# Kernel optimization log

Measured on AMD Instinct MI355X. Metric: run time of the kernel, lower is better.

Reference implementation:

```python
import jax, jax.numpy as jnp
import numpy as np
import math

L, H, P = 16384, 128, 256


def setup_inputs() -> dict:
    key = jax.random.key(0)
    k = jax.random.split(key, 6)
    return {
        "input_sequence": jax.random.normal(k[0], (L, H), dtype=jnp.float32),
        "A_diag": jax.random.uniform(k[1], (P,), dtype=jnp.float32),
        "B": (jax.random.uniform(k[2], (P, H, 2), dtype=jnp.float32) * 2.0 - 1.0) / math.sqrt(H),
        "C": (jax.random.uniform(k[3], (H, P, 2), dtype=jnp.float32) * 2.0 - 1.0) / math.sqrt(P),
        "D": jax.random.normal(k[4], (H,), dtype=jnp.float32),
        "steps": jax.random.uniform(k[5], (P,), dtype=jnp.float32),
    }


def _binop(qi, qj):
    # 2x2 block-diagonal matrix product + affine state propagation, per channel.
    iA, iB, iC, iD, ib1, ib2 = qi
    jA, jB, jC, jD, jb1, jb2 = qj
    return (
        jA * iA + jB * iC,
        jA * iB + jB * iD,
        jC * iA + jD * iC,
        jC * iB + jD * iD,
        jA * ib1 + jB * ib2 + jb1,
        jC * ib1 + jD * ib2 + jb2,
    )


def reference(input_sequence, A_diag, B, C, D, steps):
    # LinOSS-IM discretization (implicit)
    A = jax.nn.relu(A_diag)                      # (P,)
    dt = jax.nn.sigmoid(steps)                   # (P,)
    Bc = B[..., 0] + 1j * B[..., 1]              # (P,H) complex64
    Cc = C[..., 0] + 1j * C[..., 1]              # (H,P) complex64

    Bu = input_sequence @ Bc.T                   # (L,P) complex64

    schur = 1.0 / (1.0 + dt ** 2 * A)
    M11 = 1.0 - dt ** 2 * A * schur
    M12 = -dt * A * schur
    M21 = dt * schur
    M22 = schur

    ones = jnp.ones((input_sequence.shape[0], A.shape[0]), dtype=input_sequence.dtype)
    F1 = M11 * Bu * dt                           # (L,P) complex
    F2 = M21 * Bu * dt

    elems = (M11 * ones, M12 * ones, M21 * ones, M22 * ones, F1, F2)
    _, _, _, _, _, x2 = jax.lax.associative_scan(_binop, elems)  # scan over L

    ys = jnp.real(x2 @ Cc.T)                     # (L,H)
    return ys + input_sequence * D
```

## Files before the change

### kernel.cpp

```cpp
#include <hip/hip_runtime.h>
#include <math.h>

#define L 16384
#define H 128
#define P 256
#define CL 64
#define NCH (L/CL)
#define GS 16
#define NG (NCH/GS)
#define KDIM 512
#define NBU 512

typedef __attribute__((ext_vector_type(8))) short short8;
typedef __attribute__((ext_vector_type(4))) float f32x4;

__device__ inline unsigned short f2bf(float f){
  union { float f; unsigned u; } v; v.f = f;
  unsigned u = v.u;
  u += 0x7fffu + ((u >> 16) & 1u);
  return (unsigned short)(u >> 16);
}
__device__ inline float bf2f(unsigned short s){
  union { unsigned u; float f; } v; v.u = ((unsigned)s) << 16;
  return v.f;
}

struct Params { float M11,M12,M21,M22,s1,s2; };

__device__ inline Params get_params(const float* A_diag, const float* steps, int p){
  float A = A_diag[p]; A = A > 0.f ? A : 0.f;
  float dt = 1.f/(1.f + expf(-steps[p]));
  float schur = 1.f/(1.f + dt*dt*A);
  Params q;
  q.M11 = 1.f - dt*dt*A*schur;
  q.M12 = -dt*A*schur;
  q.M21 = dt*schur;
  q.M22 = schur;
  q.s1 = q.M11*dt;
  q.s2 = q.M21*dt;
  return q;
}

__device__ inline unsigned long long aload(const unsigned long long* p){
  return __hip_atomic_load((unsigned long long*)p, __ATOMIC_RELAXED,
                           __HIP_MEMORY_SCOPE_AGENT);
}
__device__ inline void apub(unsigned long long* p, unsigned long long v){
  (void)__hip_atomic_exchange(p, v, __ATOMIC_RELAXED, __HIP_MEMORY_SCOPE_AGENT);
}
__device__ inline void fpub(unsigned* p){
  (void)__hip_atomic_exchange(p, 1u, __ATOMIC_RELAXED, __HIP_MEMORY_SCOPE_AGENT);
}
__device__ inline void wait_flag(unsigned* f){
  while (__hip_atomic_load(f, __ATOMIC_RELAXED, __HIP_MEMORY_SCOPE_AGENT) == 0u)
    __builtin_amdgcn_s_sleep(1);
}

__global__ __launch_bounds__(512) void prep_w(const float* __restrict__ B,
                                              const float* __restrict__ Cw,
                                              unsigned short* __restrict__ BWswz,
                                              unsigned short* __restrict__ Bswz,
                                              unsigned* __restrict__ flags){
  int gidx = blockIdx.x*512 + threadIdx.x;
  if (gidx < NCH + NG) flags[gidx] = 0u;
  if (gidx < H*NBU){
    int k = gidx >> 9, n = gidx & 511;
    int p = n & 255, c2 = n >> 8;
    float v = B[((size_t)p*H + k)*2 + c2];
    BWswz[((size_t)(k>>3)*NBU + n)*8 + (k&7)] = f2bf(v);
  } else {
    int g2 = gidx - H*NBU;
    int k = g2 >> 7, n = g2 & 127;
    float v = (k < P) ? Cw[((size_t)n*P + k)*2]
                      : -Cw[((size_t)n*P + (k-P))*2 + 1];
    Bswz[((size_t)(k>>3)*H + n)*8 + (k&7)] = f2bf(v);
  }
}

__global__ __launch_bounds__(512, 2) void linoss_fused(
    const float* __restrict__ in,
    const float* __restrict__ A_diag,
    const float* __restrict__ steps,
    const float* __restrict__ Dv,
    const unsigned short* __restrict__ BWswz,
    const unsigned short* __restrict__ Bswz,
    unsigned long long* __restrict__ finals,
    unsigned long long* __restrict__ gfin,
    unsigned* __restrict__ flag1,
    unsigned* __restrict__ flag2,
    float* __restrict__ out)
{
  __shared__ unsigned short sX[CL][NBU+8];
  const int c   = blockIdx.x;
  const int tid = threadIdx.x;

  {
    int lane = tid & 63, w = tid >> 6;
    int ml = lane & 15, quad = lane >> 4;
    int rt = w & 3, ch = w >> 2;
    int lm0 = rt*16;
    const float* aptr = in + (size_t)(c*CL + lm0 + ml)*H + quad*8;
    short8 av[4];
    #pragma unroll
    for (int ks=0; ks<4; ks++){
      float4 f0 = *(const float4*)(aptr + ks*32);
      float4 f1 = *(const float4*)(aptr + ks*32 + 4);
      union { short8 s; unsigned short u[8]; } o;
      o.u[0]=f2bf(f0.x); o.u[1]=f2bf(f0.y); o.u[2]=f2bf(f0.z); o.u[3]=f2bf(f0.w);
      o.u[4]=f2bf(f1.x); o.u[5]=f2bf(f1.y); o.u[6]=f2bf(f1.z); o.u[7]=f2bf(f1.w);
      av[ks] = o.s;
    }
    f32x4 acc[16];
    #pragma unroll
    for (int t=0;t<16;t++) acc[t] = (f32x4){0.f,0.f,0.f,0.f};
    #pragma unroll
    for (int ks=0; ks<4; ks++){
      #pragma unroll
      for (int t=0;t<16;t++){
        int n0 = ch*256 + t*16;
        short8 bv = *(const short8*)(BWswz + ((size_t)(ks*4+quad)*NBU + n0 + ml)*8);
        acc[t] = __builtin_amdgcn_mfma_f32_16x16x32_bf16(av[ks], bv, acc[t], 0, 0, 0);
      }
    }
    #pragma unroll
    for (int t=0;t<16;t++){
      int n = ch*256 + t*16 + ml;
      #pragma unroll
      for (int r=0;r<4;r++)
        sX[lm0 + quad*4 + r][n] = f2bf(acc[t][r]);
    }
  }
  __syncthreads();

  const int p = tid & 255, part = tid >> 8;
  Params q = get_params(A_diag, steps, p);
  float Ta=q.M11, Tb=q.M12, Tc=q.M21, Td=q.M22;
  #pragma unroll
  for (int s=0;s<6;s++){
    float na=Ta*Ta+Tb*Tc, nb=Ta*Tb+Tb*Td, nc=Tc*Ta+Td*Tc, nd=Tc*Tb+Td*Td;
    Ta=na;Tb=nb;Tc=nc;Td=nd;
  }
  float fx1=0.f, fx2=0.f;
  {
    #pragma unroll
    for (int i=0;i<CL;i++){
      float u = bf2f(sX[i][part*256 + p]);
      float n1 = q.M11*fx1 + q.M12*fx2 + q.s1*u;
      float n2 = q.M21*fx1 + q.M22*fx2 + q.s2*u;
      fx1 = n1; fx2 = n2;
    }
    union { unsigned long long u; float2 f; } w; w.f = make_float2(fx1,fx2);
    apub(&finals[(size_t)(part*NCH + c)*P + p], w.u);
  }
  asm volatile("s_waitcnt vmcnt(0)" ::: "memory");
  __syncthreads();
  if (tid == 0) fpub(&flag1[c]);

  const int g = c >> 4, iw = c & (GS-1);
  const unsigned long long* Fp = finals + (size_t)part*NCH*P + (size_t)g*GS*P + p;

  float z1=0.f, z2v=0.f;
  bool have_z = false;
  if (iw == GS-1){
    if (tid < GS-1) wait_flag(&flag1[g*GS + tid]);
    __syncthreads();
    unsigned long long v[GS-1];
    #pragma unroll
    for (int j=0;j<GS-1;j++) v[j] = aload(Fp + (size_t)j*P);
    #pragma unroll
    for (int j=0;j<GS-1;j++){
      union { unsigned long long u; float2 f; } w; w.u = v[j];
      float n1 = Ta*z1 + Tb*z2v + w.f.x;
      float n2 = Tc*z1 + Td*z2v + w.f.y;
      z1=n1; z2v=n2;
    }
    have_z = true;
    float t1 = Ta*z1 + Tb*z2v + fx1;
    float t2 = Tc*z1 + Td*z2v + fx2;
    union { unsigned long long u; float2 f; } w; w.f = make_float2(t1,t2);
    apub(&gfin[(size_t)(part*NG + g)*P + p], w.u);
    asm volatile("s_waitcnt vmcnt(0)" ::: "memory");
    __syncthreads();
    if (tid == 0) fpub(&flag2[g]);
  }

  float sa=1.f, sb=0.f, sc=0.f, sd=1.f;
  {
    float wa=Ta, wb=Tb, wc=Tc, wd=Td;
    #pragma unroll
    for (int bit=0; bit<4; bit++){
      if ((iw>>bit)&1){
        float na = wa*sa + wb*sc, nb = wa*sb + wb*sd;
        float nc = wc*sa + wd*sc, nd = wc*sb + wd*sd;
        sa=na; sb=nb; sc=nc; sd=nd;
      }
      float qa = wa*wa + wb*wc, qb = wa*wb + wb*wd;
      float qc = wc*wa + wd*wc, qd = wc*wb + wd*wd;
      wa=qa; wb=qb; wc=qc; wd=qd;
    }
  }
  float ga=Ta, gb=Tb, gc=Tc, gd=Td;
  #pragma unroll
  for (int s=0;s<4;s++){
    float na=ga*ga+gb*gc, nb=ga*gb+gb*gd, nc=gc*ga+gd*gc, nd=gc*gb+gd*gd;
    ga=na;gb=nb;gc=nc;gd=nd;
  }

  if (tid < g)                             wait_flag(&flag2[tid]);
  if (!have_z && tid >= 64 && tid < 64+iw) wait_flag(&flag1[g*GS + (tid-64)]);
  __syncthreads();

  {
    const unsigned long long* Gp = gfin + (size_t)part*NG*P + p;
    unsigned long long vy[NG-1], vm[GS-1];
    #pragma unroll
    for (int j=0;j<NG-1;j++) vy[j] = (j < g) ? aload(Gp + (size_t)j*P) : 0ULL;
    if (!have_z){
      #pragma unroll
      for (int j=0;j<GS-1;j++) vm[j] = (j < iw) ? aload(Fp + (size_t)j*P) : 0ULL;
    }
    float y1=0.f, y2=0.f;
    #pragma unroll
    for (int j=0;j<NG-1;j++){
      if (j < g){
        union { unsigned long long u; float2 f; } w; w.u = vy[j];
        float n1 = ga*y1 + gb*y2 + w.f.x;
        float n2 = gc*y1 + gd*y2 + w.f.y;
        y1=n1; y2=n2;
      }
    }
    if (!have_z){
      #pragma unroll
      for (int j=0;j<GS-1;j++){
        if (j < iw){
          union { unsigned long long u; float2 f; } w; w.u = vm[j];
          float n1 = Ta*z1 + Tb*z2v + w.f.x;
          float n2 = Tc*z1 + Td*z2v + w.f.y;
          z1=n1; z2v=n2;
        }
      }
    }
    float x1 = sa*y1 + sb*y2 + z1;
    float x2 = sc*y1 + sd*y2 + z2v;
    #pragma unroll
    for (int i=0;i<CL;i++){
      float u = bf2f(sX[i][part*256 + p]);
      float n1 = q.M11*x1 + q.M12*x2 + q.s1*u;
      float n2 = q.M21*x1 + q.M22*x2 + q.s2*u;
      x1 = n1; x2 = n2;
      sX[i][part*256 + p] = f2bf(x2);
    }
  }
  __syncthreads();

  {
    int lane = tid & 63, w = tid >> 6;
    int ml = lane & 15, quad = lane >> 4;
    int rt2 = w & 3;
    int nh  = w >> 2;
    f32x4 acc[4];
    #pragma unroll
    for (int j=0;j<4;j++) acc[j] = (f32x4){0.f,0.f,0.f,0.f};
    for (int ks=0; ks<KDIM/32; ks++){
      short8 av = *(const short8*)&sX[rt2*16 + ml][ks*32 + quad*8];
      #pragma unroll
      for (int j=0;j<4;j++){
        short8 bv = *(const short8*)(Bswz + ((size_t)(ks*4+quad)*H + (nh*4+j)*16 + ml)*8);
        acc[j] = __builtin_amdgcn_mfma_f32_16x16x32_bf16(av, bv, acc[j], 0, 0, 0);
      }
    }
    #pragma unroll
    for (int j=0;j<4;j++){
      int h = (nh*4+j)*16 + ml;
      float dv = Dv[h];
      #pragma unroll
      for (int r=0;r<4;r++){
        int l = c*CL + rt2*16 + quad*4 + r;
        out[(size_t)l*H + h] = acc[j][r] + in[(size_t)l*H + h]*dv;
      }
    }
  }
}

extern "C" void kernel_launch(void* const* d_in, const int* in_sizes, int n_in,
                              void* d_out, int out_size, void* d_ws, size_t ws_size,
                              hipStream_t stream) {
  const float* in     = (const float*)d_in[0];
  const float* A_diag = (const float*)d_in[1];
  const float* B      = (const float*)d_in[2];
  const float* Cw     = (const float*)d_in[3];
  const float* Dv     = (const float*)d_in[4];
  const float* steps  = (const float*)d_in[5];
  float* out = (float*)d_out;

  unsigned short* BWswz = (unsigned short*)d_ws;
  unsigned short* Bswz  = BWswz + (size_t)H*NBU;
  unsigned long long* finals = (unsigned long long*)(Bswz + (size_t)KDIM*H);
  unsigned long long* gfin   = finals + (size_t)2*NCH*P;
  unsigned* flags = (unsigned*)(gfin + (size_t)2*NG*P);
  unsigned* flag1 = flags;
  unsigned* flag2 = flags + NCH;

  prep_w<<<256, 512, 0, stream>>>(B, Cw, BWswz, Bswz, flags);
  linoss_fused<<<NCH, 512, 0, stream>>>(in, A_diag, steps, Dv, BWswz, Bswz,
                                        finals, gfin, flag1, flag2, out);
}
```

Measured before the change: 94.36 us.

## Split fused scan kernel into two launches, replacing inter-block flag synchronization

Replaces the single persistent kernel, which coordinated chunk carries through atomic flags and a two-level group scan, with two kernels. The first computes Bu via MFMA, writes it to global memory as bf16 along with per-chunk final states. The second reloads Bu, serially folds all previous chunk finals (linear in chunk index) to get its carry-in, then rescans and projects. This removes spin-waits and flag traffic but adds an extra launch, a round trip of an 8MB Bu buffer through memory, and O(NCH) serial carry work for late blocks.

```diff
diff --git a/kernel.cpp b/kernel.cpp
--- a/kernel.cpp
+++ b/kernel.cpp
@@ -6,8 +6,6 @@
 #define P 256
 #define CL 64
 #define NCH (L/CL)
-#define GS 16
-#define NG (NCH/GS)
 #define KDIM 512
 #define NBU 512
 
@@ -41,28 +39,11 @@
   return q;
 }
 
-__device__ inline unsigned long long aload(const unsigned long long* p){
-  return __hip_atomic_load((unsigned long long*)p, __ATOMIC_RELAXED,
-                           __HIP_MEMORY_SCOPE_AGENT);
-}
-__device__ inline void apub(unsigned long long* p, unsigned long long v){
-  (void)__hip_atomic_exchange(p, v, __ATOMIC_RELAXED, __HIP_MEMORY_SCOPE_AGENT);
-}
-__device__ inline void fpub(unsigned* p){
-  (void)__hip_atomic_exchange(p, 1u, __ATOMIC_RELAXED, __HIP_MEMORY_SCOPE_AGENT);
-}
-__device__ inline void wait_flag(unsigned* f){
-  while (__hip_atomic_load(f, __ATOMIC_RELAXED, __HIP_MEMORY_SCOPE_AGENT) == 0u)
-    __builtin_amdgcn_s_sleep(1);
-}
-
 __global__ __launch_bounds__(512) void prep_w(const float* __restrict__ B,
                                               const float* __restrict__ Cw,
                                               unsigned short* __restrict__ BWswz,
-                                              unsigned short* __restrict__ Bswz,
-                                              unsigned* __restrict__ flags){
+                                              unsigned short* __restrict__ Bswz){
   int gidx = blockIdx.x*512 + threadIdx.x;
-  if (gidx < NCH + NG) flags[gidx] = 0u;
   if (gidx < H*NBU){
     int k = gidx >> 9, n = gidx & 511;
     int p = n & 255, c2 = n >> 8;
@@ -77,18 +58,13 @@
   }
 }
 
-__global__ __launch_bounds__(512, 2) void linoss_fused(
+__global__ __launch_bounds__(512, 2) void k1_bu(
     const float* __restrict__ in,
     const float* __restrict__ A_diag,
     const float* __restrict__ steps,
-    const float* __restrict__ Dv,
     const unsigned short* __restrict__ BWswz,
-    const unsigned short* __restrict__ Bswz,
-    unsigned long long* __restrict__ finals,
-    unsigned long long* __restrict__ gfin,
-    unsigned* __restrict__ flag1,
-    unsigned* __restrict__ flag2,
-    float* __restrict__ out)
+    unsigned short* __restrict__ Bu,
+    float* __restrict__ finals)
 {
   __shared__ unsigned short sX[CL][NBU+8];
   const int c   = blockIdx.x;
@@ -132,6 +108,51 @@
   }
   __syncthreads();
 
+  {
+    int row = tid >> 3, seg = tid & 7;
+    const short8* src = (const short8*)&sX[row][seg*64];
+    short8* dst = (short8*)(Bu + ((size_t)(c*CL + row)*NBU + seg*64));
+    #pragma unroll
+    for (int j=0;j<8;j++) dst[j] = src[j];
+  }
+
+  {
+    const int p = tid & 255, part = tid >> 8;
+    Params q = get_params(A_diag, steps, p);
+    float fx1=0.f, fx2=0.f;
+    #pragma unroll
+    for (int i=0;i<CL;i++){
+      float u = bf2f(sX[i][part*256 + p]);
+      float n1 = q.M11*fx1 + q.M12*fx2 + q.s1*u;
+      float n2 = q.M21*fx1 + q.M22*fx2 + q.s2*u;
+      fx1 = n1; fx2 = n2;
+    }
+    ((float2*)finals)[(size_t)(part*NCH + c)*P + p] = make_float2(fx1,fx2);
+  }
+}
+
+__global__ __launch_bounds__(512, 2) void k2_out(
+    const float* __restrict__ in,
+    const float* __restrict__ A_diag,
+    const float* __restrict__ steps,
+    const float* __restrict__ Dv,
+    const unsigned short* __restrict__ Bswz,
+    const unsigned short* __restrict__ Bu,
+    const float* __restrict__ finals,
+    float* __restrict__ out)
+{
+  __shared__ unsigned short sX[CL][NBU+8];
+  const int c   = blockIdx.x;
+  const int tid = threadIdx.x;
+
+  const int row = tid >> 3, seg = tid & 7;
+  short8 st[8];
+  {
+    const short8* src = (const short8*)(Bu + ((size_t)(c*CL + row)*NBU + seg*64));
+    #pragma unroll
+    for (int j=0;j<8;j++) st[j] = src[j];
+  }
+
   const int p = tid & 255, part = tid >> 8;
   Params q = get_params(A_diag, steps, p);
   float Ta=q.M11, Tb=q.M12, Tc=q.M21, Td=q.M22;
@@ -140,108 +161,36 @@
     float na=Ta*Ta+Tb*Tc, nb=Ta*Tb+Tb*Td, nc=Tc*Ta+Td*Tc, nd=Tc*Tb+Td*Td;
     Ta=na;Tb=nb;Tc=nc;Td=nd;
   }
-  float fx1=0.f, fx2=0.f;
-  {
-    #pragma unroll
-    for (int i=0;i<CL;i++){
-      float u = bf2f(sX[i][part*256 + p]);
-      float n1 = q.M11*fx1 + q.M12*fx2 + q.s1*u;
-      float n2 = q.M21*fx1 + q.M22*fx2 + q.s2*u;
-      fx1 = n1; fx2 = n2;
-    }
-    union { unsigned long long u; float2 f; } w; w.f = make_float2(fx1,fx2);
-    apub(&finals[(size_t)(part*NCH + c)*P + p], w.u);
-  }
-  asm volatile("s_waitcnt vmcnt(0)" ::: "memory");
+  float x1=0.f, x2=0.f;
+  {
+    const float2* F = (const float2*)finals + (size_t)part*NCH*P + p;
+    for (int t0=0; t0<c; t0+=8){
+      float2 v[8];
+      #pragma unroll
+      for (int j=0;j<8;j++){
+        int jj = t0+j;
+        v[j] = (jj < c) ? F[(size_t)jj*P] : make_float2(0.f,0.f);
+      }
+      #pragma unroll
+      for (int j=0;j<8;j++){
+        int jj = t0+j;
+        if (jj < c){
+          float n1 = Ta*x1 + Tb*x2 + v[j].x;
+          float n2 = Tc*x1 + Td*x2 + v[j].y;
+          x1=n1; x2=n2;
+        }
+      }
+    }
+  }
+
+  {
+    short8* dstl = (short8*)&sX[row][seg*64];
+    #pragma unroll
+    for (int j=0;j<8;j++) dstl[j] = st[j];
+  }
   __syncthreads();
-  if (tid == 0) fpub(&flag1[c]);
-
-  const int g = c >> 4, iw = c & (GS-1);
-  const unsigned long long* Fp = finals + (size_t)part*NCH*P + (size_t)g*GS*P + p;
-
-  float z1=0.f, z2v=0.f;
-  bool have_z = false;
-  if (iw == GS-1){
-    if (tid < GS-1) wait_flag(&flag1[g*GS + tid]);
-    __syncthreads();
-    unsigned long long v[GS-1];
-    #pragma unroll
-    for (int j=0;j<GS-1;j++) v[j] = aload(Fp + (size_t)j*P);
-    #pragma unroll
-    for (int j=0;j<GS-1;j++){
-      union { unsigned long long u; float2 f; } w; w.u = v[j];
-      float n1 = Ta*z1 + Tb*z2v + w.f.x;
-      float n2 = Tc*z1 + Td*z2v + w.f.y;
-      z1=n1; z2v=n2;
-    }
-    have_z = true;
-    float t1 = Ta*z1 + Tb*z2v + fx1;
-    float t2 = Tc*z1 + Td*z2v + fx2;
-    union { unsigned long long u; float2 f; } w; w.f = make_float2(t1,t2);
-    apub(&gfin[(size_t)(part*NG + g)*P + p], w.u);
-    asm volatile("s_waitcnt vmcnt(0)" ::: "memory");
-    __syncthreads();
-    if (tid == 0) fpub(&flag2[g]);
-  }
-
-  float sa=1.f, sb=0.f, sc=0.f, sd=1.f;
-  {
-    float wa=Ta, wb=Tb, wc=Tc, wd=Td;
-    #pragma unroll
-    for (int bit=0; bit<4; bit++){
-      if ((iw>>bit)&1){
-        float na = wa*sa + wb*sc, nb = wa*sb + wb*sd;
-        float nc = wc*sa + wd*sc, nd = wc*sb + wd*sd;
-        sa=na; sb=nb; sc=nc; sd=nd;
-      }
-      float qa = wa*wa + wb*wc, qb = wa*wb + wb*wd;
-      float qc = wc*wa + wd*wc, qd = wc*wb + wd*wd;
-      wa=qa; wb=qb; wc=qc; wd=qd;
-    }
-  }
-  float ga=Ta, gb=Tb, gc=Tc, gd=Td;
-  #pragma unroll
-  for (int s=0;s<4;s++){
-    float na=ga*ga+gb*gc, nb=ga*gb+gb*gd, nc=gc*ga+gd*gc, nd=gc*gb+gd*gd;
-    ga=na;gb=nb;gc=nc;gd=nd;
-  }
-
-  if (tid < g)                             wait_flag(&flag2[tid]);
-  if (!have_z && tid >= 64 && tid < 64+iw) wait_flag(&flag1[g*GS + (tid-64)]);
-  __syncthreads();
-
-  {
-    const unsigned long long* Gp = gfin + (size_t)part*NG*P + p;
-    unsigned long long vy[NG-1], vm[GS-1];
-    #pragma unroll
-    for (int j=0;j<NG-1;j++) vy[j] = (j < g) ? aload(Gp + (size_t)j*P) : 0ULL;
-    if (!have_z){
-      #pragma unroll
-      for (int j=0;j<GS-1;j++) vm[j] = (j < iw) ? aload(Fp + (size_t)j*P) : 0ULL;
-    }
-    float y1=0.f, y2=0.f;
-    #pragma unroll
-    for (int j=0;j<NG-1;j++){
-      if (j < g){
-        union { unsigned long long u; float2 f; } w; w.u = vy[j];
-        float n1 = ga*y1 + gb*y2 + w.f.x;
-        float n2 = gc*y1 + gd*y2 + w.f.y;
-        y1=n1; y2=n2;
-      }
-    }
-    if (!have_z){
-      #pragma unroll
-      for (int j=0;j<GS-1;j++){
-        if (j < iw){
-          union { unsigned long long u; float2 f; } w; w.u = vm[j];
-          float n1 = Ta*z1 + Tb*z2v + w.f.x;
-          float n2 = Tc*z1 + Td*z2v + w.f.y;
-          z1=n1; z2v=n2;
-        }
-      }
-    }
-    float x1 = sa*y1 + sb*y2 + z1;
-    float x2 = sc*y1 + sd*y2 + z2v;
+
+  {
     #pragma unroll
     for (int i=0;i<CL;i++){
       float u = bf2f(sX[i][part*256 + p]);
@@ -295,13 +244,10 @@
 
   unsigned short* BWswz = (unsigned short*)d_ws;
   unsigned short* Bswz  = BWswz + (size_t)H*NBU;
-  unsigned long long* finals = (unsigned long long*)(Bswz + (size_t)KDIM*H);
-  unsigned long long* gfin   = finals + (size_t)2*NCH*P;
-  unsigned* flags = (unsigned*)(gfin + (size_t)2*NG*P);
-  unsigned* flag1 = flags;
-  unsigned* flag2 = flags + NCH;
-
-  prep_w<<<256, 512, 0, stream>>>(B, Cw, BWswz, Bswz, flags);
-  linoss_fused<<<NCH, 512, 0, stream>>>(in, A_diag, steps, Dv, BWswz, Bswz,
-                                        finals, gfin, flag1, flag2, out);
-}
+  unsigned short* Bu    = Bswz + (size_t)KDIM*H;
+  float* finals = (float*)(Bu + (size_t)L*NBU);
+
+  prep_w<<<256, 512, 0, stream>>>(B, Cw, BWswz, Bswz);
+  k1_bu <<<NCH, 512, 0, stream>>>(in, A_diag, steps, BWswz, Bu, finals);
+  k2_out<<<NCH, 512, 0, stream>>>(in, A_diag, steps, Dv, Bswz, Bu, finals, out);
+}
```

Result: slower. 158.2 us (+67.6%).
